# Optimization experiments

Measured on AMD Instinct MI355X. Metric: run time of the kernel, lower is better.

The kernel has to match this reference:

```python
import jax, jax.numpy as jnp
import numpy as np

# ---- static config (mirrors DRR.__init__ kwargs) ----
NX = NY = NZ = 192            # volume dims
H = W = 192                   # detector height/width
SDR = 300.0                   # source-to-rotation-center distance
DELX = DELY = 2.0             # detector pixel pitch (mm)
X0 = Y0 = 0.0                 # detector offsets
SPACING = (1.0, 1.0, 1.0)     # voxel spacing (mm)
BAM = 1.0                     # bone_attenuation_multiplier
B = 2                         # batch (poses)
N_SUB = H * W // 2            # p_subsample = 0.5


def setup_inputs() -> dict:
    key = jax.random.key(0)
    k1, k2, k3, k4 = jax.random.split(key, 4)
    # CT volume in Hounsfield units, spanning air (-1000) to bone (~2000)
    volume = jax.random.uniform(k1, (NX, NY, NZ), jnp.float32, -1000.0, 2000.0)
    rotations = jax.random.normal(k2, (B, 3), jnp.float32)          # Euler ZYX (rad)
    translations = jax.random.normal(k3, (B, 3), jnp.float32) * 10.0  # mm, near isocenter
    # unique subsampled detector pixel indices (Detector.subsamples[-1])
    subsample_idx = jax.random.permutation(k4, H * W)[:N_SUB].astype(jnp.int32)
    return {"volume": volume, "rotations": rotations,
            "translations": translations, "subsample_idx": subsample_idx}


def _rz(t):
    c, s = jnp.cos(t), jnp.sin(t); z = jnp.zeros_like(t); o = jnp.ones_like(t)
    return jnp.stack([jnp.stack([c, -s, z], -1),
                      jnp.stack([s, c, z], -1),
                      jnp.stack([z, z, o], -1)], -2)


def _ry(t):
    c, s = jnp.cos(t), jnp.sin(t); z = jnp.zeros_like(t); o = jnp.ones_like(t)
    return jnp.stack([jnp.stack([c, z, s], -1),
                      jnp.stack([z, o, z], -1),
                      jnp.stack([-s, z, c], -1)], -2)


def _rx(t):
    c, s = jnp.cos(t), jnp.sin(t); z = jnp.zeros_like(t); o = jnp.ones_like(t)
    return jnp.stack([jnp.stack([o, z, z], -1),
                      jnp.stack([z, c, -s], -1),
                      jnp.stack([z, s, c], -1)], -2)


def _density(volume):
    # DRR.__init__: volume.flip([0]); air/soft/bone HU segmentation + normalization
    vol = jnp.flip(volume, 0)
    soft = (vol > -800.0) & (vol <= 350.0)
    soft_min = jnp.min(jnp.where(soft, vol, jnp.inf))
    d = jnp.where(vol <= -800.0, soft_min,
                  jnp.where(vol > 350.0, vol * BAM, vol))
    d = d - jnp.min(d)
    return d / jnp.max(d)


def _canonical_detector():
    # source on +z at SDR, detector plane at -z; pixel grid with pitch delx/dely
    xs = (jnp.arange(W, dtype=jnp.float32) - (W - 1) / 2.0) * DELX + X0
    ys = (jnp.arange(H, dtype=jnp.float32) - (H - 1) / 2.0) * DELY + Y0
    gy, gx = jnp.meshgrid(ys, xs, indexing="ij")
    tgt = jnp.stack([gx.ravel(), gy.ravel(),
                     jnp.full((H * W,), -SDR, jnp.float32)], -1)  # [H*W, 3]
    src = jnp.array([0.0, 0.0, SDR], jnp.float32)
    return src, tgt


def _siddon(density, source, target):
    """Siddon ray-casting. source [B,3], target [B,N,3] -> line integrals [B,N]."""
    dims = density.shape
    sp = jnp.asarray(SPACING, density.dtype)
    src = source[:, None, :]                     # [B,1,3]
    sdd = target - src                           # [B,N,3]
    sdd_safe = jnp.where(sdd == 0, 1e-9, sdd)
    # parametric intersections with all grid planes per axis
    alist = [(jnp.arange(dims[a] + 1, dtype=density.dtype)[None, None, :] * sp[a]
              - src[..., a:a + 1]) / sdd_safe[..., a:a + 1] for a in range(3)]
    a_first = jnp.stack([al[..., 0] for al in alist], -1)    # [B,N,3]
    a_last = jnp.stack([al[..., -1] for al in alist], -1)
    amin = jnp.maximum(jnp.max(jnp.minimum(a_first, a_last), -1), 0.0)[..., None]
    amax = jnp.minimum(jnp.min(jnp.maximum(a_first, a_last), -1), 1.0)[..., None]
    amax = jnp.maximum(amax, amin)               # ray misses -> zero-length segments
    alphas = jnp.sort(jnp.clip(jnp.concatenate(alist, -1), amin, amax), -1)  # [B,N,M+1]
    mid = 0.5 * (alphas[..., 1:] + alphas[..., :-1])                         # [B,N,M]
    ray_len = jnp.linalg.norm(target - src, axis=-1, keepdims=True)
    step = (alphas[..., 1:] - alphas[..., :-1]) * ray_len                    # [B,N,M]
    pts = src[..., None, :] + mid[..., None] * sdd[..., None, :]             # [B,N,M,3]
    idx = jnp.clip(jnp.floor(pts / sp).astype(jnp.int32), 0,
                   jnp.array(dims, jnp.int32) - 1)
    vox = density[idx[..., 0], idx[..., 1], idx[..., 2]]                     # gather
    return jnp.sum(step * vox, -1)


def reference(volume, rotations, translations, subsample_idx):
    density = _density(volume)
    src_c, tgt_c = _canonical_detector()
    tgt_c = tgt_c[subsample_idx]                                  # [N,3] subsampled rays
    R = _rz(rotations[:, 0]) @ _ry(rotations[:, 1]) @ _rx(rotations[:, 2])  # [B,3,3]
    center = jnp.array([NX, NY, NZ], jnp.float32) * jnp.asarray(SPACING, jnp.float32) / 2.0
    t = translations + center                                     # pose about isocenter
    source = jnp.einsum("bij,j->bi", R, src_c) + t                # [B,3]
    target = jnp.einsum("bij,nj->bni", R, tgt_c) + t[:, None, :]  # [B,N,3]
    img = _siddon(density, source, target)                        # [B,N]
    # reshape_subsampled_drr: scatter into zeros [B, H*W] then view [B,1,H,W]
    drr = jnp.zeros((img.shape[0], H * W), img.dtype).at[:, subsample_idx].set(img)
    return drr.reshape(-1, 1, H, W)
```

## Files before the change

kernel.cpp:

```cpp
#include <hip/hip_runtime.h>
#include <float.h>
#include <math.h>


#define NDIM   192
#define HW     (NDIM * NDIM)
#define NSUB   (HW / 2)
#define NTILE  576
#define NBATCH 2
#define NCHUNK 16
#define NVOX   (NDIM * NDIM * NDIM)
#define SDRF   300.0f
#define RBLK   1728

#define WS_MARK_OFF 16
#define WS_LIST_OFF (16 + HW)
#define WS_CNT_OFF  (WS_LIST_OFF + 4 * NSUB)
#define WS_OFF_OFF  (WS_CNT_OFF + 4 * NTILE)
#define WS_PART_OFF (WS_OFF_OFF + 4 * NTILE)

__global__ __launch_bounds__(256) void reduce_kernel(
    const float* __restrict__ vol, float* __restrict__ parts) {
    const int tid = blockIdx.x * 256 + threadIdx.x;
    const float4* __restrict__ v4 = (const float4*)vol;
    const int S = RBLK * 256;

    float4 r0 = v4[tid + 0 * S];
    float4 r1 = v4[tid + 1 * S];
    float4 r2 = v4[tid + 2 * S];
    float4 r3 = v4[tid + 3 * S];

    float smin = FLT_MAX, rmin = FLT_MAX, rmax = -FLT_MAX;
    float4 rr[4] = {r0, r1, r2, r3};
#pragma unroll
    for (int k = 0; k < 4; ++k) {
        float xs[4] = {rr[k].x, rr[k].y, rr[k].z, rr[k].w};
#pragma unroll
        for (int j = 0; j < 4; ++j) {
            float x = xs[j];
            bool in = (x > -800.0f);
            rmin = fminf(rmin, in ? x : FLT_MAX);
            rmax = fmaxf(rmax, in ? x : -FLT_MAX);
            smin = fminf(smin, (in && x <= 350.0f) ? x : FLT_MAX);
        }
    }
#pragma unroll
    for (int off = 32; off > 0; off >>= 1) {
        smin = fminf(smin, __shfl_down(smin, off));
        rmin = fminf(rmin, __shfl_down(rmin, off));
        rmax = fmaxf(rmax, __shfl_down(rmax, off));
    }
    __shared__ float sm[4], rm[4], rx[4];
    int w = threadIdx.x >> 6;
    if ((threadIdx.x & 63) == 0) { sm[w] = smin; rm[w] = rmin; rx[w] = rmax; }
    __syncthreads();
    if (threadIdx.x == 0) {
        parts[blockIdx.x] =
            fminf(fminf(sm[0], sm[1]), fminf(sm[2], sm[3]));
        parts[RBLK + blockIdx.x] =
            fminf(fminf(rm[0], rm[1]), fminf(rm[2], rm[3]));
        parts[2 * RBLK + blockIdx.x] =
            fmaxf(fmaxf(rx[0], rx[1]), fmaxf(rx[2], rx[3]));
    }
}

__global__ __launch_bounds__(256) void reduce_final(
    const float* __restrict__ parts, float* __restrict__ ws) {
    float smin = FLT_MAX, rmin = FLT_MAX, rmax = -FLT_MAX;
    for (int i = threadIdx.x; i < RBLK; i += 256) {
        smin = fminf(smin, parts[i]);
        rmin = fminf(rmin, parts[RBLK + i]);
        rmax = fmaxf(rmax, parts[2 * RBLK + i]);
    }
#pragma unroll
    for (int off = 32; off > 0; off >>= 1) {
        smin = fminf(smin, __shfl_down(smin, off));
        rmin = fminf(rmin, __shfl_down(rmin, off));
        rmax = fmaxf(rmax, __shfl_down(rmax, off));
    }
    __shared__ float sm[4], rm[4], rx[4];
    int w = threadIdx.x >> 6;
    if ((threadIdx.x & 63) == 0) { sm[w] = smin; rm[w] = rmin; rx[w] = rmax; }
    __syncthreads();
    if (threadIdx.x == 0) {
        ws[0] = fminf(fminf(sm[0], sm[1]), fminf(sm[2], sm[3]));
        ws[1] = fminf(fminf(rm[0], rm[1]), fminf(rm[2], rm[3]));
        ws[2] = fmaxf(fmaxf(rx[0], rx[1]), fmaxf(rx[2], rx[3]));
    }
}

__global__ __launch_bounds__(256) void scatter_mark(
    const int* __restrict__ idx, unsigned char* __restrict__ mark) {
    int n = blockIdx.x * blockDim.x + threadIdx.x;
    if (n < NSUB) mark[idx[n]] = 1;
}

__device__ __forceinline__ int key_to_pixel(int tile, int lane) {
    int pi = (tile / 24) * 8 + (lane >> 3);
    int pj = (tile % 24) * 8 + (lane & 7);
    return pi * NDIM + pj;
}

__global__ __launch_bounds__(256) void count_kernel(
    const unsigned char* __restrict__ mark, int* __restrict__ counts) {
    int lane = threadIdx.x & 63;
    int tile = blockIdx.x * 4 + (threadIdx.x >> 6);
    int p = key_to_pixel(tile, lane);
    unsigned long long mask = __ballot(mark[p] != 0);
    if (lane == 0) counts[tile] = __popcll(mask);
}

__global__ __launch_bounds__(NTILE) void scan_kernel(
    const int* __restrict__ counts, int* __restrict__ offs) {
    __shared__ int s[NTILE];
    int t = threadIdx.x;
    int c = counts[t];
    s[t] = c;
    __syncthreads();
    for (int off = 1; off < NTILE; off <<= 1) {
        int v = s[t];
        int u = (t >= off) ? s[t - off] : 0;
        __syncthreads();
        s[t] = v + u;
        __syncthreads();
    }
    offs[t] = s[t] - c;
}

__global__ __launch_bounds__(256) void emit_kernel(
    const unsigned char* __restrict__ mark, const int* __restrict__ offs,
    int* __restrict__ list) {
    int lane = threadIdx.x & 63;
    int tile = blockIdx.x * 4 + (threadIdx.x >> 6);
    int p = key_to_pixel(tile, lane);
    bool m = (mark[p] != 0);
    unsigned long long mask = __ballot(m);
    int rank = __popcll(mask & ((1ull << lane) - 1ull));
    if (m) list[offs[tile] + rank] = p;
}

__device__ __forceinline__ void init_axis(float s, float d, float a_lo,
                                          int& i, int& st, float& na) {
    if (d > 0.0f) {
        st = 1;
        float f = s + a_lo * d;
        int ii = (int)floorf(f) + 1;
        ii = max(0, min(ii, NDIM + 1));
        while (ii <= NDIM && ((float)ii - s) / d <= a_lo) ++ii;
        while (ii > 0 && ((float)(ii - 1) - s) / d > a_lo) --ii;
        i  = ii;
        na = (ii <= NDIM) ? ((float)ii - s) / d : FLT_MAX;
    } else {
        st = -1;
        float f = s + a_lo * d;
        int ii = (int)ceilf(f) - 1;
        ii = max(-1, min(ii, NDIM));
        while (ii >= 0 && ((float)ii - s) / d <= a_lo) --ii;
        while (ii < NDIM && ((float)(ii + 1) - s) / d > a_lo) ++ii;
        i  = ii;
        na = (ii >= 0) ? ((float)ii - s) / d : FLT_MAX;
    }
}

__global__ __launch_bounds__(256) void ray_kernel(
    const float* __restrict__ vol, const float* __restrict__ rot,
    const float* __restrict__ trans, const float* __restrict__ wsc,
    const int* __restrict__ list, float* __restrict__ out) {
    const int n = blockIdx.x * 256 + threadIdx.x;
    const int c = blockIdx.y;
    const int b = blockIdx.z;

    const int p  = list[n];
    const int pi = p / NDIM;
    const int pj = p % NDIM;

    float smin = wsc[0];
    float rmin = wsc[1];
    float rmax = wsc[2];
    float dmin = fminf(smin, rmin);
    float dmax = fmaxf(smin, rmax);
    float scale = 1.0f / (dmax - dmin);

    float rz = rot[b * 3 + 0], ry = rot[b * 3 + 1], rx = rot[b * 3 + 2];
    float cz = cosf(rz), sz = sinf(rz);
    float cy = cosf(ry), sy = sinf(ry);
    float cx = cosf(rx), sx = sinf(rx);
    float R00 = cz * cy;
    float R01 = cz * sy * sx - sz * cx;
    float R02 = sz * sx + cz * sy * cx;
    float R10 = sz * cy;
    float R11 = cz * cx + sz * sy * sx;
    float R12 = sz * sy * cx - cz * sx;
    float R20 = -sy;
    float R21 = cy * sx;
    float R22 = cy * cx;
    float tx = trans[b * 3 + 0] + 96.0f;
    float ty = trans[b * 3 + 1] + 96.0f;
    float tz = trans[b * 3 + 2] + 96.0f;

    float srcx = R02 * SDRF + tx;
    float srcy = R12 * SDRF + ty;
    float srcz = R22 * SDRF + tz;
    float gx = ((float)pj - 95.5f) * 2.0f;
    float gy = ((float)pi - 95.5f) * 2.0f;
    float tgx = R00 * gx + R01 * gy + R02 * (-SDRF) + tx;
    float tgy = R10 * gx + R11 * gy + R12 * (-SDRF) + ty;
    float tgz = R20 * gx + R21 * gy + R22 * (-SDRF) + tz;

    float sdx = tgx - srcx, sdy = tgy - srcy, sdz = tgz - srcz;
    float dsx = (sdx == 0.0f) ? 1e-9f : sdx;
    float dsy = (sdy == 0.0f) ? 1e-9f : sdy;
    float dsz = (sdz == 0.0f) ? 1e-9f : sdz;

    float af0 = (0.0f - srcx) / dsx, al0 = (192.0f - srcx) / dsx;
    float af1 = (0.0f - srcy) / dsy, al1 = (192.0f - srcy) / dsy;
    float af2 = (0.0f - srcz) / dsz, al2 = (192.0f - srcz) / dsz;
    float amin = fmaxf(fmaxf(fminf(af0, al0), fminf(af1, al1)), fminf(af2, al2));
    amin = fmaxf(amin, 0.0f);
    float amax = fminf(fminf(fmaxf(af0, al0), fmaxf(af1, al1)), fmaxf(af2, al2));
    amax = fminf(amax, 1.0f);
    amax = fmaxf(amax, amin);
    float ray_len = sqrtf(sdx * sdx + sdy * sdy + sdz * sdz);

    float span = amax - amin;
    float a_lo = amin + span * ((float)c / (float)NCHUNK);
    float a_hi = (c == NCHUNK - 1) ? amax
                                   : amin + span * ((float)(c + 1) / (float)NCHUNK);

    int i0, i1, i2, st0, st1, st2;
    float na0, na1, na2;
    init_axis(srcx, dsx, a_lo, i0, st0, na0);
    init_axis(srcy, dsy, a_lo, i1, st1, na1);
    init_axis(srcz, dsz, a_lo, i2, st2, na2);

    float r0 = 1.0f / dsx, r1 = 1.0f / dsy, r2 = 1.0f / dsz;
    float fi0 = (float)i0, fi1 = (float)i1, fi2 = (float)i2;
    float fs0 = (float)st0, fs1 = (float)st1, fs2 = (float)st2;

    float cur = a_lo;
    float acc = 0.0f;
    while (true) {
        float an  = fminf(fminf(na0, na1), na2);
        bool fin  = !(an < a_hi);
        float a2  = fin ? a_hi : an;
        float mid = 0.5f * (cur + a2);
        float px = fmaf(mid, sdx, srcx);
        float py = fmaf(mid, sdy, srcy);
        float pz = fmaf(mid, sdz, srcz);
        int ix = min(max((int)px, 0), NDIM - 1);
        int iy = min(max((int)py, 0), NDIM - 1);
        int iz = min(max((int)pz, 0), NDIM - 1);
        int addr = (NDIM - 1) * HW - ix * HW + iy * NDIM + iz;
        float v  = vol[addr];
        float dv = (v <= -800.0f) ? smin : v;
        acc = fmaf(a2 - cur, dv, acc);
        if (fin) break;
        cur = a2;
        bool c0 = (na0 == an), c1 = (na1 == an), c2 = (na2 == an);
        float nf0 = fi0 + fs0, nf1 = fi1 + fs1, nf2 = fi2 + fs2;
        float nn0 = (nf0 - srcx) * r0;
        float nn1 = (nf1 - srcy) * r1;
        float nn2 = (nf2 - srcz) * r2;
        fi0 = c0 ? nf0 : fi0;  na0 = c0 ? nn0 : na0;
        fi1 = c1 ? nf1 : fi1;  na1 = c1 ? nn1 : na1;
        fi2 = c2 ? nf2 : fi2;  na2 = c2 ? nn2 : na2;
    }
    float res = (acc - dmin * (a_hi - a_lo)) * scale * ray_len;
    atomicAdd(&out[b * HW + p], res);
}

extern "C" void kernel_launch(void* const* d_in, const int* in_sizes, int n_in,
                              void* d_out, int out_size, void* d_ws,
                              size_t ws_size, hipStream_t stream) {
    const float* vol   = (const float*)d_in[0];
    const float* rot   = (const float*)d_in[1];
    const float* trans = (const float*)d_in[2];
    const int*   sidx  = (const int*)d_in[3];
    float* out = (float*)d_out;

    float*         wsf    = (float*)d_ws;
    unsigned char* mark   = (unsigned char*)d_ws + WS_MARK_OFF;
    int*           list   = (int*)((unsigned char*)d_ws + WS_LIST_OFF);
    int*           counts = (int*)((unsigned char*)d_ws + WS_CNT_OFF);
    int*           offs   = (int*)((unsigned char*)d_ws + WS_OFF_OFF);
    float*         parts  = (float*)((unsigned char*)d_ws + WS_PART_OFF);

    hipMemsetAsync(d_out, 0, (size_t)out_size * sizeof(float), stream);
    hipMemsetAsync(mark, 0, HW, stream);

    reduce_kernel<<<RBLK, 256, 0, stream>>>(vol, parts);
    reduce_final<<<1, 256, 0, stream>>>(parts, wsf);
    scatter_mark<<<NSUB / 256, 256, 0, stream>>>(sidx, mark);
    count_kernel<<<NTILE / 4, 256, 0, stream>>>(mark, counts);
    scan_kernel<<<1, NTILE, 0, stream>>>(counts, offs);
    emit_kernel<<<NTILE / 4, 256, 0, stream>>>(mark, offs, list);
    dim3 rgrid(NSUB / 256, NCHUNK, NBATCH);
    ray_kernel<<<rgrid, 256, 0, stream>>>(vol, rot, trans, wsf, list, out);
}
```

Baseline: 127.9 us.

## Fuse final reduction, marking, count, scan and emit into one prep kernel

Replaces five small kernels and a memset (reduce_final, scatter_mark, count, scan, emit) with a single 1024-thread block that builds a shared-memory bitmask of subsampled pixels, counts per 8x8 tile, scans, and emits the sorted pixel list. This removes several launch gaps and global round trips for the mark and count arrays. The cost is that all of this work now runs serially on one block, including 18432 shared atomicOr operations and a per-thread serial emit loop.

```diff
diff --git a/kernel.cpp b/kernel.cpp
--- a/kernel.cpp
+++ b/kernel.cpp
@@ -13,11 +13,8 @@
 #define SDRF   300.0f
 #define RBLK   1728
 
-#define WS_MARK_OFF 16
-#define WS_LIST_OFF (16 + HW)
-#define WS_CNT_OFF  (WS_LIST_OFF + 4 * NSUB)
-#define WS_OFF_OFF  (WS_CNT_OFF + 4 * NTILE)
-#define WS_PART_OFF (WS_OFF_OFF + 4 * NTILE)
+#define WS_LIST_OFF 16
+#define WS_PART_OFF (WS_LIST_OFF + 4 * NSUB)
 
 __global__ __launch_bounds__(256) void reduce_kernel(
     const float* __restrict__ vol, float* __restrict__ parts) {
@@ -64,10 +61,17 @@
     }
 }
 
-__global__ __launch_bounds__(256) void reduce_final(
-    const float* __restrict__ parts, float* __restrict__ ws) {
+__global__ __launch_bounds__(1024) void prep_kernel(
+    const float* __restrict__ parts, const int* __restrict__ sidx,
+    float* __restrict__ ws, int* __restrict__ list) {
+    __shared__ unsigned int bits[HW / 32];
+    __shared__ int cnts[NTILE];
+    __shared__ float red0[16], red1[16], red2[16];
+
+    const int tid = threadIdx.x;
+
     float smin = FLT_MAX, rmin = FLT_MAX, rmax = -FLT_MAX;
-    for (int i = threadIdx.x; i < RBLK; i += 256) {
+    for (int i = tid; i < RBLK; i += 1024) {
         smin = fminf(smin, parts[i]);
         rmin = fminf(rmin, parts[RBLK + i]);
         rmax = fmaxf(rmax, parts[2 * RBLK + i]);
@@ -78,65 +82,63 @@
         rmin = fminf(rmin, __shfl_down(rmin, off));
         rmax = fmaxf(rmax, __shfl_down(rmax, off));
     }
-    __shared__ float sm[4], rm[4], rx[4];
-    int w = threadIdx.x >> 6;
-    if ((threadIdx.x & 63) == 0) { sm[w] = smin; rm[w] = rmin; rx[w] = rmax; }
-    __syncthreads();
-    if (threadIdx.x == 0) {
-        ws[0] = fminf(fminf(sm[0], sm[1]), fminf(sm[2], sm[3]));
-        ws[1] = fminf(fminf(rm[0], rm[1]), fminf(rm[2], rm[3]));
-        ws[2] = fmaxf(fmaxf(rx[0], rx[1]), fmaxf(rx[2], rx[3]));
-    }
-}
-
-__global__ __launch_bounds__(256) void scatter_mark(
-    const int* __restrict__ idx, unsigned char* __restrict__ mark) {
-    int n = blockIdx.x * blockDim.x + threadIdx.x;
-    if (n < NSUB) mark[idx[n]] = 1;
-}
-
-__device__ __forceinline__ int key_to_pixel(int tile, int lane) {
-    int pi = (tile / 24) * 8 + (lane >> 3);
-    int pj = (tile % 24) * 8 + (lane & 7);
-    return pi * NDIM + pj;
-}
-
-__global__ __launch_bounds__(256) void count_kernel(
-    const unsigned char* __restrict__ mark, int* __restrict__ counts) {
-    int lane = threadIdx.x & 63;
-    int tile = blockIdx.x * 4 + (threadIdx.x >> 6);
-    int p = key_to_pixel(tile, lane);
-    unsigned long long mask = __ballot(mark[p] != 0);
-    if (lane == 0) counts[tile] = __popcll(mask);
-}
-
-__global__ __launch_bounds__(NTILE) void scan_kernel(
-    const int* __restrict__ counts, int* __restrict__ offs) {
-    __shared__ int s[NTILE];
-    int t = threadIdx.x;
-    int c = counts[t];
-    s[t] = c;
-    __syncthreads();
+    int w = tid >> 6;
+    if ((tid & 63) == 0) { red0[w] = smin; red1[w] = rmin; red2[w] = rmax; }
+
+    for (int i = tid; i < HW / 32; i += 1024) bits[i] = 0u;
+    __syncthreads();
+    if (tid == 0) {
+        float a = FLT_MAX, b = FLT_MAX, c = -FLT_MAX;
+#pragma unroll
+        for (int k = 0; k < 16; ++k) {
+            a = fminf(a, red0[k]);
+            b = fminf(b, red1[k]);
+            c = fmaxf(c, red2[k]);
+        }
+        ws[0] = a; ws[1] = b; ws[2] = c;
+    }
+
+    for (int i = tid; i < NSUB; i += 1024) {
+        int p = sidx[i];
+        atomicOr(&bits[p >> 5], 1u << (p & 31));
+    }
+    __syncthreads();
+
+    const unsigned char* bb = (const unsigned char*)bits;
+    int myc = 0;
+    int ti = tid / 24, tj = tid % 24;
+    if (tid < NTILE) {
+#pragma unroll
+        for (int r = 0; r < 8; ++r)
+            myc += __popc((int)bb[(ti * 8 + r) * 24 + tj]);
+        cnts[tid] = myc;
+    }
+    __syncthreads();
+
     for (int off = 1; off < NTILE; off <<= 1) {
-        int v = s[t];
-        int u = (t >= off) ? s[t - off] : 0;
+        int v = 0, u = 0;
+        if (tid < NTILE) {
+            v = cnts[tid];
+            if (tid >= off) u = cnts[tid - off];
+        }
         __syncthreads();
-        s[t] = v + u;
+        if (tid < NTILE) cnts[tid] = v + u;
         __syncthreads();
     }
-    offs[t] = s[t] - c;
-}
-
-__global__ __launch_bounds__(256) void emit_kernel(
-    const unsigned char* __restrict__ mark, const int* __restrict__ offs,
-    int* __restrict__ list) {
-    int lane = threadIdx.x & 63;
-    int tile = blockIdx.x * 4 + (threadIdx.x >> 6);
-    int p = key_to_pixel(tile, lane);
-    bool m = (mark[p] != 0);
-    unsigned long long mask = __ballot(m);
-    int rank = __popcll(mask & ((1ull << lane) - 1ull));
-    if (m) list[offs[tile] + rank] = p;
+
+    if (tid < NTILE) {
+        int o = cnts[tid] - myc;
+#pragma unroll
+        for (int r = 0; r < 8; ++r) {
+            int pibase = (ti * 8 + r) * NDIM + tj * 8;
+            unsigned int m = (unsigned int)bb[(ti * 8 + r) * 24 + tj];
+            while (m) {
+                int j = __ffs(m) - 1;
+                m &= m - 1u;
+                list[o++] = pibase + j;
+            }
+        }
+    }
 }
 
 __device__ __forceinline__ void init_axis(float s, float d, float a_lo,
@@ -278,22 +280,14 @@
     const int*   sidx  = (const int*)d_in[3];
     float* out = (float*)d_out;
 
-    float*         wsf    = (float*)d_ws;
-    unsigned char* mark   = (unsigned char*)d_ws + WS_MARK_OFF;
-    int*           list   = (int*)((unsigned char*)d_ws + WS_LIST_OFF);
-    int*           counts = (int*)((unsigned char*)d_ws + WS_CNT_OFF);
-    int*           offs   = (int*)((unsigned char*)d_ws + WS_OFF_OFF);
-    float*         parts  = (float*)((unsigned char*)d_ws + WS_PART_OFF);
+    float* wsf   = (float*)d_ws;
+    int*   list  = (int*)((unsigned char*)d_ws + WS_LIST_OFF);
+    float* parts = (float*)((unsigned char*)d_ws + WS_PART_OFF);
 
     hipMemsetAsync(d_out, 0, (size_t)out_size * sizeof(float), stream);
-    hipMemsetAsync(mark, 0, HW, stream);
 
     reduce_kernel<<<RBLK, 256, 0, stream>>>(vol, parts);
-    reduce_final<<<1, 256, 0, stream>>>(parts, wsf);
-    scatter_mark<<<NSUB / 256, 256, 0, stream>>>(sidx, mark);
-    count_kernel<<<NTILE / 4, 256, 0, stream>>>(mark, counts);
-    scan_kernel<<<1, NTILE, 0, stream>>>(counts, offs);
-    emit_kernel<<<NTILE / 4, 256, 0, stream>>>(mark, offs, list);
+    prep_kernel<<<1, 1024, 0, stream>>>(parts, sidx, wsf, list);
     dim3 rgrid(NSUB / 256, NCHUNK, NBATCH);
     ray_kernel<<<rgrid, 256, 0, stream>>>(vol, rot, trans, wsf, list, out);
 }
```

Result: slower. 132.2 us (+3.4%).
